# Performance work log

Measured on AMD Instinct MI355X. Metric: run time of the kernel, lower is better.

## Reference

```python
import jax, jax.numpy as jnp
import numpy as np

B, C, H, W = 4, 64, 64, 64
DK, DV = 64, 64


def _conv1x1(x, w, b):
    # x: [B,C,H,W], w: [O,C], b: [O] -> [B,O,H,W]
    return jnp.einsum('bchw,oc->bohw', x, w) + b[None, :, None, None]


def _ordered_mask(N, ordering, dtype):
    mask = jnp.tril(jnp.ones((N, N), dtype=dtype))
    if ordering == 1:
        return mask
    elif ordering == 2:
        return jnp.flip(mask, 1)
    elif ordering == 3:
        return jnp.rot90(mask, 1)
    elif ordering == 4:
        return jnp.flip(jnp.rot90(mask, 1), 0)
    elif ordering == 5:
        return jnp.rot90(mask, 2)
    elif ordering == 6:
        return jnp.flip(jnp.rot90(mask, 2), 1)
    elif ordering == 7:
        return jnp.rot90(mask, 3)
    elif ordering == 8:
        return jnp.flip(jnp.rot90(mask, 3), 1)
    return None


def setup_inputs() -> dict:
    key = jax.random.key(0)
    ks = jax.random.split(key, 9)
    s = 0.02
    return {
        'x': jax.random.normal(ks[0], (B, C, H, W), dtype=jnp.float32),
        'Wq': jax.random.normal(ks[1], (DK, C), dtype=jnp.float32) * s,
        'bq': jnp.zeros((DK,), dtype=jnp.float32),
        'Wk': jax.random.normal(ks[2], (DK, C), dtype=jnp.float32) * s,
        'bk': jnp.zeros((DK,), dtype=jnp.float32),
        'Wv': jax.random.normal(ks[3], (DV, C), dtype=jnp.float32) * s,
        'bv': jnp.zeros((DV,), dtype=jnp.float32),
        'Wo': jax.random.normal(ks[4], (DV, DV + C), dtype=jnp.float32) * s,
        'bo': jnp.zeros((DV,), dtype=jnp.float32),
        'ordering': 1,
    }


def reference(x, Wq, bq, Wk, bk, Wv, bv, Wo, bo, ordering):
    b, c, h, w = x.shape
    N = h * w
    dk, dv = Wq.shape[0], Wv.shape[0]
    Q = _conv1x1(x, Wq, bq).reshape(b, dk, N)  # [B,dk,N]
    K = _conv1x1(x, Wk, bk).reshape(b, dk, N)  # [B,dk,N]
    V = _conv1x1(x, Wv, bv).reshape(b, dv, N)  # [B,dv,N]
    logits = jnp.einsum('bdn,bdm->bnm', Q, K)  # [B,N,N] (no 1/sqrt(dk) scaling, matching source)
    weights = jax.nn.softmax(logits, axis=-1)
    m = _ordered_mask(N, ordering, x.dtype)
    if m is not None:
        weights = weights * m  # post-softmax multiplicative mask
    o = jnp.einsum('bnm,bdm->bdn', weights, V).reshape(b, dv, h, w)
    oc = jnp.concatenate([o, x], axis=1)  # [B,dv+C,H,W]
    return _conv1x1(oc, Wo, bo)
```

## Files before the change

kernel.cpp:

```cpp
#include <hip/hip_runtime.h>

typedef __attribute__((ext_vector_type(8))) short short8;
typedef __attribute__((ext_vector_type(4))) short short4v;
typedef __attribute__((ext_vector_type(4))) float f32x4;
typedef __attribute__((ext_vector_type(16))) float f32x16;
typedef __attribute__((ext_vector_type(4))) unsigned int uint4v;
typedef __attribute__((ext_vector_type(2))) unsigned int uint2v;
typedef unsigned short us;
typedef unsigned int u32;

#define NB 4
#define NC 64
#define NN 4096
#define ND 64
#define LOG2E 1.44269504088896340736f

static __device__ __forceinline__ us f2bf(float x) {
    u32 u = __builtin_bit_cast(u32, x);
    u += 0x7FFFu + ((u >> 16) & 1u);
    return (us)(u >> 16);
}

static __device__ __forceinline__ float bf2f(us v) {
    u32 u = ((u32)v) << 16;
    return __builtin_bit_cast(float, u);
}

static __device__ __forceinline__ u32 cvtpk(float a, float b) {
    u32 r;
    asm("v_cvt_pk_bf16_f32 %0, %1, %2" : "=v"(r) : "v"(a), "v"(b));
    return r;
}

static __device__ __forceinline__ short8 comb(short4v a, short4v b) {
    short8 r;
    r[0] = a[0]; r[1] = a[1]; r[2] = a[2]; r[3] = a[3];
    r[4] = b[0]; r[5] = b[1]; r[6] = b[2]; r[7] = b[3];
    return r;
}

static __device__ __forceinline__ void async_copy16(void* lds, const void* g) {
    __builtin_amdgcn_global_load_lds(
        (const __attribute__((address_space(1))) u32*)g,
        (__attribute__((address_space(3))) u32*)lds, 16, 0, 0);
}

static __device__ __forceinline__ int swz8(int row) {
    return (row & 7) ^ ((row >> 3) & 3);
}

__global__ void cvt_kernel(const float* __restrict__ Wo,
                           const float* __restrict__ Wq,
                           const float* __restrict__ Wk,
                           const float* __restrict__ Wv,
                           us* __restrict__ Wob, us* __restrict__ Wqb,
                           us* __restrict__ Wkb, us* __restrict__ Wvb) {
    int i = blockIdx.x * 256 + threadIdx.x;
    if (i < 8192) Wob[i] = f2bf(Wo[i]);
    else if (i < 12288) Wqb[i - 8192] = f2bf(Wq[i - 8192] * LOG2E);
    else if (i < 16384) Wkb[i - 12288] = f2bf(Wk[i - 12288]);
    else if (i < 20480) Wvb[i - 16384] = f2bf(Wv[i - 16384]);
}

__global__ __launch_bounds__(256) void proj_kernel(
    const float* __restrict__ x,
    const us* __restrict__ Wqb, const float* __restrict__ bq,
    const us* __restrict__ Wkb, const float* __restrict__ bk,
    const us* __restrict__ Wvb, const float* __restrict__ bv,
    us* __restrict__ Qt, us* __restrict__ Kt,
    us* __restrict__ Vm, us* __restrict__ Xbt)
{
    __shared__ float xs[64][64];
    __shared__ __align__(16) us xT[64][64];
    const int t = threadIdx.x;
    const int bid = blockIdx.x;
    const int role = bid & 1;
    const int v = bid >> 1;
    const int b = v >> 6;
    const int n0 = (v & 63) << 6;
    const float* xb = x + (size_t)b * NC * NN + n0;
    #pragma unroll
    for (int i = 0; i < 4; ++i) {
        int s = t + i * 256;
        int c = s >> 4, col = (s & 15) << 2;
        *(f32x4*)&xs[c][col] = *(const f32x4*)&xb[(size_t)c * NN + col];
    }
    __syncthreads();
    {
        int n = t & 63, cg = t >> 6;
        int c0 = cg << 4;
        u32 pk[8];
        #pragma unroll
        for (int j = 0; j < 8; ++j) {
            float a0 = xs[c0 + 2 * j][n], a1 = xs[c0 + 2 * j + 1][n];
            pk[j] = (u32)f2bf(a0) | ((u32)f2bf(a1) << 16);
        }
        int b0 = (cg * 2) ^ (n & 7), b1 = (cg * 2 + 1) ^ (n & 7);
        *(uint4v*)&xT[n][b0 * 8] = (uint4v){pk[0], pk[1], pk[2], pk[3]};
        *(uint4v*)&xT[n][b1 * 8] = (uint4v){pk[4], pk[5], pk[6], pk[7]};
        if (role == 1) {
            us* dst = Xbt + (size_t)(b * NN + n0 + n) * ND + c0;
            *(uint4v*)dst       = (uint4v){pk[0], pk[1], pk[2], pk[3]};
            *(uint4v*)(dst + 8) = (uint4v){pk[4], pk[5], pk[6], pk[7]};
        }
    }
    __syncthreads();
    const int w = t >> 6, l = t & 63, h = l >> 4, ln = l & 15;
    const int row = w * 16 + ln;
    short8 xq0 = *(const short8*)&xT[row][((h ^ (row & 7)) << 3)];
    short8 xq1 = *(const short8*)&xT[row][(((4 + h) ^ (row & 7)) << 3)];

    if (role == 0) {
        #pragma unroll
        for (int p = 0; p < 2; ++p) {
            const us* Wb = p ? Wkb : Wqb;
            const float* bias = p ? bk : bq;
            const float sc = p ? 1.0f : LOG2E;
            us* outp = p ? Kt : Qt;
            #pragma unroll
            for (int di = 0; di < 4; ++di) {
                const int d = di * 16 + ln;
                const us* wrb = Wb + (size_t)d * 64;
                short8 a0 = *(const short8*)(wrb + h * 8);
                short8 a1 = *(const short8*)(wrb + 32 + h * 8);
                f32x4 acc = *(const f32x4*)(bias + di * 16 + h * 4);
                acc *= sc;
                acc = __builtin_amdgcn_mfma_f32_16x16x32_bf16(a0, xq0, acc, 0, 0, 0);
                acc = __builtin_amdgcn_mfma_f32_16x16x32_bf16(a1, xq1, acc, 0, 0, 0);
                u32 lo = (u32)f2bf(acc[0]) | ((u32)f2bf(acc[1]) << 16);
                u32 hi2 = (u32)f2bf(acc[2]) | ((u32)f2bf(acc[3]) << 16);
                *(uint2v*)(outp + (size_t)(b * NN + n0 + row) * ND + di * 16 + h * 4) = (uint2v){lo, hi2};
            }
        }
    } else {
        #pragma unroll
        for (int di = 0; di < 4; ++di) {
            const int d = di * 16 + ln;
            const us* wrb = Wvb + (size_t)d * 64;
            short8 a0 = *(const short8*)(wrb + h * 8);
            short8 a1 = *(const short8*)(wrb + 32 + h * 8);
            f32x4 acc = *(const f32x4*)(bv + di * 16 + h * 4);
            acc = __builtin_amdgcn_mfma_f32_16x16x32_bf16(a0, xq0, acc, 0, 0, 0);
            acc = __builtin_amdgcn_mfma_f32_16x16x32_bf16(a1, xq1, acc, 0, 0, 0);
            us* vp = Vm + (size_t)(b * ND + di * 16 + h * 4) * NN + n0 + row;
            vp[0] = f2bf(acc[0]); vp[NN] = f2bf(acc[1]);
            vp[2 * NN] = f2bf(acc[2]); vp[3 * NN] = f2bf(acc[3]);
        }
    }
}

static __device__ __forceinline__ void mask_bounds32(int pt, int n032, int ng,
    int& lo_n, int& hi_n, int& lo_min, int& lo_max, int& hi_min, int& hi_max)
{
    if (pt == 0)      { lo_n = 0;           hi_n = ng;          lo_min = 0;              lo_max = 0;             hi_min = n032;           hi_max = n032 + 31; }
    else if (pt == 1) { lo_n = NN - 1 - ng; hi_n = NN - 1;      lo_min = NN - 32 - n032; lo_max = NN - 1 - n032; hi_min = NN - 1;         hi_max = NN - 1; }
    else if (pt == 2) { lo_n = ng;          hi_n = NN - 1;      lo_min = n032;           lo_max = n032 + 31;     hi_min = NN - 1;         hi_max = NN - 1; }
    else if (pt == 3) { lo_n = 0;           hi_n = NN - 1 - ng; lo_min = 0;              lo_max = 0;             hi_min = NN - 32 - n032; hi_max = NN - 1 - n032; }
    else              { lo_n = 0;           hi_n = NN - 1;      lo_min = 0;              lo_max = 0;             hi_min = NN - 1;         hi_max = NN - 1; }
}

__global__ __launch_bounds__(512, 4) void attn_kernel(
    const us* __restrict__ Qt, const us* __restrict__ Kt,
    const us* __restrict__ Vm,
    const int* __restrict__ ordp,
    u32* __restrict__ Opk, float* __restrict__ Lb)
{
    __shared__ __align__(16) us Kl[2][64 * 64];
    __shared__ __align__(16) us Vl[2][64 * 64];
    __shared__ float cL[128];

    const int tid = threadIdx.x;
    const int w = tid >> 6, l = tid & 63;
    const int hi = l >> 5, ln = l & 31;
    const int nh = w & 3, mh = w >> 2;
    const int bid = blockIdx.x;
    const int vid = (bid & 7) * 64 + (bid >> 3);
    const int b = vid >> 7;
    const int ms = (vid >> 5) & 3;
    const int qt = vid & 31;
    const int n0 = qt << 7;
    const int mbase = ms << 10;
    const int n032 = n0 + nh * 32;
    const int ng = n032 + ln;

    const int ord = ordp[0];
    int pt = 4;
    if (ord == 1) pt = 0;
    else if (ord == 2 || ord == 3) pt = 1;
    else if (ord == 4 || ord == 5 || ord == 8) pt = 2;
    else if (ord == 6 || ord == 7) pt = 3;
    int lo_n, hi_n, lo_min, lo_max, hi_min, hi_max;
    mask_bounds32(pt, n032, ng, lo_n, hi_n, lo_min, lo_max, hi_min, hi_max);

    const us* kb = Kt + (size_t)b * NN * ND;
    const us* vb = Vm + (size_t)b * ND * NN;
    const us* qrow = Qt + (size_t)(b * NN + n032 + ln) * ND;
    short8 qf0 = *(const short8*)(qrow + 0 * 16 + hi * 8);
    short8 qf1 = *(const short8*)(qrow + 1 * 16 + hi * 8);
    short8 qf2 = *(const short8*)(qrow + 2 * 16 + hi * 8);
    short8 qf3 = *(const short8*)(qrow + 3 * 16 + hi * 8);

    f32x16 O0, O1, Z;
    #pragma unroll
    for (int i = 0; i < 16; ++i) { O0[i] = 0.f; O1[i] = 0.f; Z[i] = 0.f; }
    float Lp = 0.f;

    auto stage = [&](int buf, int t) {
        const int m_base = mbase + t * 64;
        if (w < 4) {
            #pragma unroll
            for (int r = 0; r < 2; ++r) {
                const int rl = w * 16 + r * 8 + (l >> 3);
                const int blk = l & 7;
                const us* src = kb + (size_t)(m_base + rl) * ND + ((blk ^ swz8(rl)) << 3);
                async_copy16(&Kl[buf][(w * 16 + r * 8) * 64], src);
            }
        } else {
            #pragma unroll
            for (int r = 0; r < 2; ++r) {
                const int rl = (w - 4) * 16 + r * 8 + (l >> 3);
                const int blk = l & 7;
                const us* src = vb + (size_t)rl * NN + m_base + ((blk ^ swz8(rl)) << 3);
                async_copy16(&Vl[buf][((w - 4) * 16 + r * 8) * 64], src);
            }
        }
    };

    stage(0, 0);
    for (int t = 0; t < 16; ++t) {
        if (t < 15) {
            stage((t + 1) & 1, t + 1);
            asm volatile("s_waitcnt vmcnt(2)" ::: "memory");
        } else {
            asm volatile("s_waitcnt vmcnt(0)" ::: "memory");
        }
        __builtin_amdgcn_s_barrier();
        __builtin_amdgcn_sched_barrier(0);

        const us* KT = Kl[t & 1];
        const us* VT = Vl[t & 1];
        const int m0s = mbase + t * 64 + mh * 32;
        const bool skip = (m0s + 31 < lo_min) || (m0s > hi_max);
        const bool full = (m0s >= lo_max) && (m0s + 31 <= hi_min);

        __builtin_amdgcn_s_setprio(1);
        {
            const int row = mh * 32 + ln;
            const int rs = swz8(row);
            short8 a0 = *(const short8*)&KT[row * 64 + (((0 + hi) ^ rs) << 3)];
            short8 a1 = *(const short8*)&KT[row * 64 + (((2 + hi) ^ rs) << 3)];
            short8 a2 = *(const short8*)&KT[row * 64 + (((4 + hi) ^ rs) << 3)];
            short8 a3 = *(const short8*)&KT[row * 64 + (((6 + hi) ^ rs) << 3)];
            f32x16 st = __builtin_amdgcn_mfma_f32_32x32x16_bf16(a0, qf0, Z, 0, 0, 0);
            st = __builtin_amdgcn_mfma_f32_32x32x16_bf16(a1, qf1, st, 0, 0, 0);
            st = __builtin_amdgcn_mfma_f32_32x32x16_bf16(a2, qf2, st, 0, 0, 0);
            st = __builtin_amdgcn_mfma_f32_32x32x16_bf16(a3, qf3, st, 0, 0, 0);

            float p[16];
            float lp0 = 0.f, lp1 = 0.f;
            #pragma unroll
            for (int r = 0; r < 16; ++r) {
                p[r] = __builtin_amdgcn_exp2f(st[r]);
                if (r & 1) lp1 += p[r]; else lp0 += p[r];
            }
            Lp += lp0 + lp1;
            if (!skip) {
                if (!full) {
                    #pragma unroll
                    for (int r = 0; r < 16; ++r) {
                        const int mg = m0s + (r & 3) + 8 * (r >> 2) + 4 * hi;
                        if (mg < lo_n || mg > hi_n) p[r] = 0.f;
                    }
                }
                #pragma unroll
                for (int c16 = 0; c16 < 2; ++c16) {
                    uint4v pw;
                    pw[0] = cvtpk(p[c16 * 8 + 0], p[c16 * 8 + 1]);
                    pw[1] = cvtpk(p[c16 * 8 + 2], p[c16 * 8 + 3]);
                    pw[2] = cvtpk(p[c16 * 8 + 4], p[c16 * 8 + 5]);
                    pw[3] = cvtpk(p[c16 * 8 + 6], p[c16 * 8 + 7]);
                    short8 pb = __builtin_bit_cast(short8, pw);
                    const int blkA = mh * 4 + c16 * 2;
                    {
                        const int rv = ln, rvs = swz8(rv);
                        short4v va  = *(const short4v*)&VT[rv * 64 + ((blkA ^ rvs) << 3) + hi * 4];
                        short4v vb2 = *(const short4v*)&VT[rv * 64 + (((blkA + 1) ^ rvs) << 3) + hi * 4];
                        O0 = __builtin_amdgcn_mfma_f32_32x32x16_bf16(comb(va, vb2), pb, O0, 0, 0, 0);
                    }
                    {
                        const int rv = 32 + ln, rvs = swz8(rv);
                        short4v va  = *(const short4v*)&VT[rv * 64 + ((blkA ^ rvs) << 3) + hi * 4];
                        short4v vb2 = *(const short4v*)&VT[rv * 64 + (((blkA + 1) ^ rvs) << 3) + hi * 4];
                        O1 = __builtin_amdgcn_mfma_f32_32x32x16_bf16(comb(va, vb2), pb, O1, 0, 0, 0);
                    }
                }
            }
        }
        __builtin_amdgcn_s_setprio(0);
        __builtin_amdgcn_sched_barrier(0);
        __builtin_amdgcn_s_barrier();
    }

    float Lw = Lp + __shfl_xor(Lp, 32);

    float* cO = (nh < 2 ? (float*)&Kl[0][0] : (float*)&Vl[0][0]) + (nh & 1) * 2048;
    if (mh == 1) {
        float* dsto = cO + ln * 64;
        #pragma unroll
        for (int rq = 0; rq < 4; ++rq) {
            f32x4 s0, s1;
            #pragma unroll
            for (int j = 0; j < 4; ++j) { s0[j] = O0[rq * 4 + j]; s1[j] = O1[rq * 4 + j]; }
            *(f32x4*)&dsto[rq * 8 + hi * 4] = s0;
            *(f32x4*)&dsto[32 + rq * 8 + hi * 4] = s1;
        }
        if (hi == 0) cL[nh * 32 + ln] = Lw;
    }
    __syncthreads();
    if (mh == 1) return;

    const float gL = Lw + cL[nh * 32 + ln];
    const float* sp = cO + ln * 64;
    f32x16 On0 = O0, On1 = O1;
    #pragma unroll
    for (int rq = 0; rq < 4; ++rq) {
        f32x4 a = *(const f32x4*)&sp[rq * 8 + hi * 4];
        f32x4 c = *(const f32x4*)&sp[32 + rq * 8 + hi * 4];
        #pragma unroll
        for (int j = 0; j < 4; ++j) { On0[rq * 4 + j] += a[j]; On1[rq * 4 + j] += c[j]; }
    }

    u32* opk = Opk + ((size_t)(ms * NB + b) * 32) * NN + n032 + ln;
    #pragma unroll
    for (int rp = 0; rp < 16; rp += 2) {
        const int dp = ((rp & 3) >> 1) + 4 * (rp >> 2) + 2 * hi;
        opk[(size_t)dp * NN] = cvtpk(On0[rp], On0[rp + 1]);
        opk[(size_t)(dp + 16) * NN] = cvtpk(On1[rp], On1[rp + 1]);
    }
    if (hi == 0) Lb[(size_t)(ms * NB + b) * NN + n032 + ln] = gL;
}

__global__ __launch_bounds__(64) void combine_kernel(
    const u32* __restrict__ Opk, const float* __restrict__ Lb,
    const us* __restrict__ Xbt, const us* __restrict__ Wob,
    const float* __restrict__ bo, float* __restrict__ out)
{
    const int l = threadIdx.x, hi = l >> 5, ln = l & 31;
    const int gw = blockIdx.x;
    const int b = gw >> 7;
    const int n032 = (gw & 127) << 5;
    const int q = n032 + ln;

    f32x16 On0, On1;
    #pragma unroll
    for (int i = 0; i < 16; ++i) { On0[i] = 0.f; On1[i] = 0.f; }
    #pragma unroll
    for (int part = 0; part < 4; ++part) {
        const u32* pb = Opk + ((size_t)(part * NB + b) * 32) * NN + q;
        #pragma unroll
        for (int rp = 0; rp < 16; rp += 2) {
            const int dp = ((rp & 3) >> 1) + 4 * (rp >> 2) + 2 * hi;
            u32 w0 = pb[(size_t)dp * NN];
            u32 w1 = pb[(size_t)(dp + 16) * NN];
            On0[rp]     += bf2f((us)(w0 & 0xFFFFu));
            On0[rp + 1] += bf2f((us)(w0 >> 16));
            On1[rp]     += bf2f((us)(w1 & 0xFFFFu));
            On1[rp + 1] += bf2f((us)(w1 >> 16));
        }
    }
    float gL = 0.f;
    #pragma unroll
    for (int i = 0; i < 4; ++i) gL += Lb[(size_t)(i * NB + b) * NN + q];
    const float rl2 = 1.0f / gL;
    #pragma unroll
    for (int i = 0; i < 16; ++i) { On0[i] *= rl2; On1[i] *= rl2; }

    short8 Bf[8];
    {
        uint4v w0, w1, w2, w3;
        w0[0] = cvtpk(On0[0], On0[1]);   w0[1] = cvtpk(On0[2], On0[3]);
        w0[2] = cvtpk(On0[4], On0[5]);   w0[3] = cvtpk(On0[6], On0[7]);
        w1[0] = cvtpk(On0[8], On0[9]);   w1[1] = cvtpk(On0[10], On0[11]);
        w1[2] = cvtpk(On0[12], On0[13]); w1[3] = cvtpk(On0[14], On0[15]);
        w2[0] = cvtpk(On1[0], On1[1]);   w2[1] = cvtpk(On1[2], On1[3]);
        w2[2] = cvtpk(On1[4], On1[5]);   w2[3] = cvtpk(On1[6], On1[7]);
        w3[0] = cvtpk(On1[8], On1[9]);   w3[1] = cvtpk(On1[10], On1[11]);
        w3[2] = cvtpk(On1[12], On1[13]); w3[3] = cvtpk(On1[14], On1[15]);
        Bf[0] = __builtin_bit_cast(short8, w0);
        Bf[1] = __builtin_bit_cast(short8, w1);
        Bf[2] = __builtin_bit_cast(short8, w2);
        Bf[3] = __builtin_bit_cast(short8, w3);
    }
    const us* xrow = Xbt + (size_t)(b * NN + q) * ND;
    #pragma unroll
    for (int c4 = 0; c4 < 4; ++c4)
        Bf[4 + c4] = comb(*(const short4v*)(xrow + c4 * 16 + hi * 4),
                          *(const short4v*)(xrow + c4 * 16 + hi * 4 + 8));

    f32x16 acc0, acc1;
    #pragma unroll
    for (int rq = 0; rq < 4; ++rq) {
        f32x4 b0 = *(const f32x4*)&bo[rq * 8 + hi * 4];
        f32x4 b1 = *(const f32x4*)&bo[32 + rq * 8 + hi * 4];
        #pragma unroll
        for (int j = 0; j < 4; ++j) { acc0[rq * 4 + j] = b0[j]; acc1[rq * 4 + j] = b1[j]; }
    }
    const us* wr0 = Wob + (size_t)ln * 128;
    const us* wr1 = Wob + (size_t)(32 + ln) * 128;
    #pragma unroll
    for (int kc = 0; kc < 8; ++kc) {
        short8 wf0 = comb(*(const short4v*)(wr0 + kc * 16 + hi * 4),
                          *(const short4v*)(wr0 + kc * 16 + hi * 4 + 8));
        short8 wf1 = comb(*(const short4v*)(wr1 + kc * 16 + hi * 4),
                          *(const short4v*)(wr1 + kc * 16 + hi * 4 + 8));
        acc0 = __builtin_amdgcn_mfma_f32_32x32x16_bf16(wf0, Bf[kc], acc0, 0, 0, 0);
        acc1 = __builtin_amdgcn_mfma_f32_32x32x16_bf16(wf1, Bf[kc], acc1, 0, 0, 0);
    }
    #pragma unroll
    for (int r = 0; r < 16; ++r) {
        const int od = (r & 3) + 8 * (r >> 2) + 4 * hi;
        out[((size_t)b * 64 + od) * NN + q] = acc0[r];
        out[((size_t)b * 64 + 32 + od) * NN + q] = acc1[r];
    }
}

extern "C" void kernel_launch(void* const* d_in, const int* in_sizes, int n_in,
                              void* d_out, int out_size, void* d_ws, size_t ws_size,
                              hipStream_t stream) {
    (void)in_sizes; (void)n_in; (void)out_size; (void)ws_size;
    const float* x  = (const float*)d_in[0];
    const float* Wq = (const float*)d_in[1];
    const float* bq = (const float*)d_in[2];
    const float* Wk = (const float*)d_in[3];
    const float* bk = (const float*)d_in[4];
    const float* Wv = (const float*)d_in[5];
    const float* bv = (const float*)d_in[6];
    const float* Wo = (const float*)d_in[7];
    const float* bo = (const float*)d_in[8];
    const int* ord  = (const int*)d_in[9];
    float* out = (float*)d_out;

    us* Qt  = (us*)d_ws;
    us* Kt  = Qt  + (size_t)NB * NN * ND;
    us* Vm  = Kt  + (size_t)NB * NN * ND;
    us* Xbt = Vm  + (size_t)NB * NN * ND;
    us* Wob = Xbt + (size_t)NB * NN * ND;
    u32* Opk = (u32*)(Wob + ND * (ND + NC));
    float* Lb = (float*)(Opk + (size_t)16 * 32 * NN);
    us* Wqb = (us*)(Lb + (size_t)4 * NB * NN);
    us* Wkb = Wqb + 4096;
    us* Wvb = Wkb + 4096;

    cvt_kernel<<<dim3(80), dim3(256), 0, stream>>>(Wo, Wq, Wk, Wv, Wob, Wqb, Wkb, Wvb);
    proj_kernel<<<dim3(NB * 64 * 2), dim3(256), 0, stream>>>(
        x, Wqb, bq, Wkb, bk, Wvb, bv, Qt, Kt, Vm, Xbt);
    attn_kernel<<<dim3(512), dim3(512), 0, stream>>>(Qt, Kt, Vm, ord, Opk, Lb);
    combine_kernel<<<dim3(512), dim3(64), 0, stream>>>(Opk, Lb, Xbt, Wob, bo, out);
}
```

Baseline: 52.97 us.

## Repack K/V into MFMA fragment layout and read directly from global without LDS

Adds a repack kernel that rewrites K and V into per-32-key tiles already in MFMA operand order. The attention kernel then loads fragments straight from global memory (L2-cached) instead of staging them through double-buffered LDS with barriers. Each wave now independently handles one 32-query group over one of eight key splits, which removes the intra-block LDS reduction. The combine kernel sums eight partials instead of four. The cost is an extra kernel launch, twice the partial-output traffic, and reliance on cache hits for the K/V reuse that LDS used to provide.

```diff
diff --git a/kernel.cpp b/kernel.cpp
--- a/kernel.cpp
+++ b/kernel.cpp
@@ -37,16 +37,6 @@
     r[0] = a[0]; r[1] = a[1]; r[2] = a[2]; r[3] = a[3];
     r[4] = b[0]; r[5] = b[1]; r[6] = b[2]; r[7] = b[3];
     return r;
-}
-
-static __device__ __forceinline__ void async_copy16(void* lds, const void* g) {
-    __builtin_amdgcn_global_load_lds(
-        (const __attribute__((address_space(1))) u32*)g,
-        (__attribute__((address_space(3))) u32*)lds, 16, 0, 0);
-}
-
-static __device__ __forceinline__ int swz8(int row) {
-    return (row & 7) ^ ((row >> 3) & 3);
 }
 
 __global__ void cvt_kernel(const float* __restrict__ Wo,
@@ -149,6 +139,31 @@
     }
 }
 
+__global__ __launch_bounds__(256) void repack_kernel(
+    const us* __restrict__ Kt, const us* __restrict__ Vm,
+    us* __restrict__ Kf, us* __restrict__ Vf)
+{
+    const int bid = blockIdx.x;
+    const int b = bid >> 7, mt = bid & 127;
+    const int t = threadIdx.x;
+    const int l = t & 63, s = t >> 6;
+    {
+        const int row = mt * 32 + (l & 31);
+        const int d0 = s * 16 + (l >> 5) * 8;
+        uint4v v = *(const uint4v*)(Kt + ((size_t)b * NN + row) * ND + d0);
+        *(uint4v*)(Kf + ((size_t)(b * 128 + mt) * 2048) + s * 512 + l * 8) = v;
+    }
+    {
+        const int dh = s >> 1, c16 = s & 1;
+        const int d = dh * 32 + (l & 31);
+        const int m0 = mt * 32 + c16 * 16 + (l >> 5) * 4;
+        const us* src = Vm + ((size_t)b * ND + d) * NN + m0;
+        short4v a = *(const short4v*)src;
+        short4v c = *(const short4v*)(src + 8);
+        *(short8*)(Vf + ((size_t)(b * 128 + mt) * 2048) + s * 512 + l * 8) = comb(a, c);
+    }
+}
+
 static __device__ __forceinline__ void mask_bounds32(int pt, int n032, int ng,
     int& lo_n, int& hi_n, int& lo_min, int& lo_max, int& hi_min, int& hi_max)
 {
@@ -159,29 +174,23 @@
     else              { lo_n = 0;           hi_n = NN - 1;      lo_min = 0;              lo_max = 0;             hi_min = NN - 1;         hi_max = NN - 1; }
 }
 
-__global__ __launch_bounds__(512, 4) void attn_kernel(
-    const us* __restrict__ Qt, const us* __restrict__ Kt,
-    const us* __restrict__ Vm,
+__global__ __launch_bounds__(256, 4) void attn_kernel(
+    const us* __restrict__ Qt, const us* __restrict__ Kf,
+    const us* __restrict__ Vf,
     const int* __restrict__ ordp,
     u32* __restrict__ Opk, float* __restrict__ Lb)
 {
-    __shared__ __align__(16) us Kl[2][64 * 64];
-    __shared__ __align__(16) us Vl[2][64 * 64];
-    __shared__ float cL[128];
-
     const int tid = threadIdx.x;
     const int w = tid >> 6, l = tid & 63;
     const int hi = l >> 5, ln = l & 31;
-    const int nh = w & 3, mh = w >> 2;
     const int bid = blockIdx.x;
-    const int vid = (bid & 7) * 64 + (bid >> 3);
-    const int b = vid >> 7;
-    const int ms = (vid >> 5) & 3;
-    const int qt = vid & 31;
-    const int n0 = qt << 7;
-    const int mbase = ms << 10;
-    const int n032 = n0 + nh * 32;
-    const int ng = n032 + ln;
+    const int vid = (bid & 7) * 128 + (bid >> 3);
+    const int W = vid * 4 + w;
+    const int combo = W >> 7;
+    const int b = combo >> 3, ms = combo & 7;
+    const int qg = W & 127;
+    const int q0 = qg << 5;
+    const int ng = q0 + ln;
 
     const int ord = ordp[0];
     int pt = 4;
@@ -190,11 +199,9 @@
     else if (ord == 4 || ord == 5 || ord == 8) pt = 2;
     else if (ord == 6 || ord == 7) pt = 3;
     int lo_n, hi_n, lo_min, lo_max, hi_min, hi_max;
-    mask_bounds32(pt, n032, ng, lo_n, hi_n, lo_min, lo_max, hi_min, hi_max);
-
-    const us* kb = Kt + (size_t)b * NN * ND;
-    const us* vb = Vm + (size_t)b * ND * NN;
-    const us* qrow = Qt + (size_t)(b * NN + n032 + ln) * ND;
+    mask_bounds32(pt, q0, ng, lo_n, hi_n, lo_min, lo_max, hi_min, hi_max);
+
+    const us* qrow = Qt + (size_t)(b * NN + q0 + ln) * ND;
     short8 qf0 = *(const short8*)(qrow + 0 * 16 + hi * 8);
     short8 qf1 = *(const short8*)(qrow + 1 * 16 + hi * 8);
     short8 qf2 = *(const short8*)(qrow + 2 * 16 + hi * 8);
@@ -205,139 +212,68 @@
     for (int i = 0; i < 16; ++i) { O0[i] = 0.f; O1[i] = 0.f; Z[i] = 0.f; }
     float Lp = 0.f;
 
-    auto stage = [&](int buf, int t) {
-        const int m_base = mbase + t * 64;
-        if (w < 4) {
-            #pragma unroll
-            for (int r = 0; r < 2; ++r) {
-                const int rl = w * 16 + r * 8 + (l >> 3);
-                const int blk = l & 7;
-                const us* src = kb + (size_t)(m_base + rl) * ND + ((blk ^ swz8(rl)) << 3);
-                async_copy16(&Kl[buf][(w * 16 + r * 8) * 64], src);
-            }
-        } else {
-            #pragma unroll
-            for (int r = 0; r < 2; ++r) {
-                const int rl = (w - 4) * 16 + r * 8 + (l >> 3);
-                const int blk = l & 7;
-                const us* src = vb + (size_t)rl * NN + m_base + ((blk ^ swz8(rl)) << 3);
-                async_copy16(&Vl[buf][((w - 4) * 16 + r * 8) * 64], src);
-            }
-        }
-    };
-
-    stage(0, 0);
+    const us* kfb = Kf + (size_t)(b * 128 + ms * 16) * 2048;
+    const us* vfb = Vf + (size_t)(b * 128 + ms * 16) * 2048;
+
+    #pragma unroll 2
     for (int t = 0; t < 16; ++t) {
-        if (t < 15) {
-            stage((t + 1) & 1, t + 1);
-            asm volatile("s_waitcnt vmcnt(2)" ::: "memory");
-        } else {
-            asm volatile("s_waitcnt vmcnt(0)" ::: "memory");
-        }
-        __builtin_amdgcn_s_barrier();
-        __builtin_amdgcn_sched_barrier(0);
-
-        const us* KT = Kl[t & 1];
-        const us* VT = Vl[t & 1];
-        const int m0s = mbase + t * 64 + mh * 32;
+        const us* kt = kfb + t * 2048 + l * 8;
+        short8 a0 = *(const short8*)(kt);
+        short8 a1 = *(const short8*)(kt + 512);
+        short8 a2 = *(const short8*)(kt + 1024);
+        short8 a3 = *(const short8*)(kt + 1536);
+        const int m0s = (ms * 16 + t) * 32;
         const bool skip = (m0s + 31 < lo_min) || (m0s > hi_max);
         const bool full = (m0s >= lo_max) && (m0s + 31 <= hi_min);
 
-        __builtin_amdgcn_s_setprio(1);
-        {
-            const int row = mh * 32 + ln;
-            const int rs = swz8(row);
-            short8 a0 = *(const short8*)&KT[row * 64 + (((0 + hi) ^ rs) << 3)];
-            short8 a1 = *(const short8*)&KT[row * 64 + (((2 + hi) ^ rs) << 3)];
-            short8 a2 = *(const short8*)&KT[row * 64 + (((4 + hi) ^ rs) << 3)];
-            short8 a3 = *(const short8*)&KT[row * 64 + (((6 + hi) ^ rs) << 3)];
-            f32x16 st = __builtin_amdgcn_mfma_f32_32x32x16_bf16(a0, qf0, Z, 0, 0, 0);
-            st = __builtin_amdgcn_mfma_f32_32x32x16_bf16(a1, qf1, st, 0, 0, 0);
-            st = __builtin_amdgcn_mfma_f32_32x32x16_bf16(a2, qf2, st, 0, 0, 0);
-            st = __builtin_amdgcn_mfma_f32_32x32x16_bf16(a3, qf3, st, 0, 0, 0);
-
-            float p[16];
-            float lp0 = 0.f, lp1 = 0.f;
-            #pragma unroll
-            for (int r = 0; r < 16; ++r) {
-                p[r] = __builtin_amdgcn_exp2f(st[r]);
-                if (r & 1) lp1 += p[r]; else lp0 += p[r];
-            }
-            Lp += lp0 + lp1;
-            if (!skip) {
-                if (!full) {
-                    #pragma unroll
-                    for (int r = 0; r < 16; ++r) {
-                        const int mg = m0s + (r & 3) + 8 * (r >> 2) + 4 * hi;
-                        if (mg < lo_n || mg > hi_n) p[r] = 0.f;
-                    }
-                }
+        f32x16 st = __builtin_amdgcn_mfma_f32_32x32x16_bf16(a0, qf0, Z, 0, 0, 0);
+        st = __builtin_amdgcn_mfma_f32_32x32x16_bf16(a1, qf1, st, 0, 0, 0);
+        st = __builtin_amdgcn_mfma_f32_32x32x16_bf16(a2, qf2, st, 0, 0, 0);
+        st = __builtin_amdgcn_mfma_f32_32x32x16_bf16(a3, qf3, st, 0, 0, 0);
+
+        float p[16];
+        float lp0 = 0.f, lp1 = 0.f;
+        #pragma unroll
+        for (int r = 0; r < 16; ++r) {
+            p[r] = __builtin_amdgcn_exp2f(st[r]);
+            if (r & 1) lp1 += p[r]; else lp0 += p[r];
+        }
+        Lp += lp0 + lp1;
+        if (!skip) {
+            if (!full) {
                 #pragma unroll
-                for (int c16 = 0; c16 < 2; ++c16) {
-                    uint4v pw;
-                    pw[0] = cvtpk(p[c16 * 8 + 0], p[c16 * 8 + 1]);
-                    pw[1] = cvtpk(p[c16 * 8 + 2], p[c16 * 8 + 3]);
-                    pw[2] = cvtpk(p[c16 * 8 + 4], p[c16 * 8 + 5]);
-                    pw[3] = cvtpk(p[c16 * 8 + 6], p[c16 * 8 + 7]);
-                    short8 pb = __builtin_bit_cast(short8, pw);
-                    const int blkA = mh * 4 + c16 * 2;
-                    {
-                        const int rv = ln, rvs = swz8(rv);
-                        short4v va  = *(const short4v*)&VT[rv * 64 + ((blkA ^ rvs) << 3) + hi * 4];
-                        short4v vb2 = *(const short4v*)&VT[rv * 64 + (((blkA + 1) ^ rvs) << 3) + hi * 4];
-                        O0 = __builtin_amdgcn_mfma_f32_32x32x16_bf16(comb(va, vb2), pb, O0, 0, 0, 0);
-                    }
-                    {
-                        const int rv = 32 + ln, rvs = swz8(rv);
-                        short4v va  = *(const short4v*)&VT[rv * 64 + ((blkA ^ rvs) << 3) + hi * 4];
-                        short4v vb2 = *(const short4v*)&VT[rv * 64 + (((blkA + 1) ^ rvs) << 3) + hi * 4];
-                        O1 = __builtin_amdgcn_mfma_f32_32x32x16_bf16(comb(va, vb2), pb, O1, 0, 0, 0);
-                    }
+                for (int r = 0; r < 16; ++r) {
+                    const int mg = m0s + (r & 3) + 8 * (r >> 2) + 4 * hi;
+                    if (mg < lo_n || mg > hi_n) p[r] = 0.f;
                 }
             }
-        }
-        __builtin_amdgcn_s_setprio(0);
-        __builtin_amdgcn_sched_barrier(0);
-        __builtin_amdgcn_s_barrier();
+            const us* vt = vfb + t * 2048 + l * 8;
+            #pragma unroll
+            for (int c16 = 0; c16 < 2; ++c16) {
+                uint4v pw;
+                pw[0] = cvtpk(p[c16 * 8 + 0], p[c16 * 8 + 1]);
+                pw[1] = cvtpk(p[c16 * 8 + 2], p[c16 * 8 + 3]);
+                pw[2] = cvtpk(p[c16 * 8 + 4], p[c16 * 8 + 5]);
+                pw[3] = cvtpk(p[c16 * 8 + 6], p[c16 * 8 + 7]);
+                short8 pb = __builtin_bit_cast(short8, pw);
+                short8 v0 = *(const short8*)(vt + (0 * 2 + c16) * 512);
+                short8 v1 = *(const short8*)(vt + (1 * 2 + c16) * 512);
+                O0 = __builtin_amdgcn_mfma_f32_32x32x16_bf16(v0, pb, O0, 0, 0, 0);
+                O1 = __builtin_amdgcn_mfma_f32_32x32x16_bf16(v1, pb, O1, 0, 0, 0);
+            }
+        }
     }
 
     float Lw = Lp + __shfl_xor(Lp, 32);
 
-    float* cO = (nh < 2 ? (float*)&Kl[0][0] : (float*)&Vl[0][0]) + (nh & 1) * 2048;
-    if (mh == 1) {
-        float* dsto = cO + ln * 64;
-        #pragma unroll
-        for (int rq = 0; rq < 4; ++rq) {
-            f32x4 s0, s1;
-            #pragma unroll
-            for (int j = 0; j < 4; ++j) { s0[j] = O0[rq * 4 + j]; s1[j] = O1[rq * 4 + j]; }
-            *(f32x4*)&dsto[rq * 8 + hi * 4] = s0;
-            *(f32x4*)&dsto[32 + rq * 8 + hi * 4] = s1;
-        }
-        if (hi == 0) cL[nh * 32 + ln] = Lw;
-    }
-    __syncthreads();
-    if (mh == 1) return;
-
-    const float gL = Lw + cL[nh * 32 + ln];
-    const float* sp = cO + ln * 64;
-    f32x16 On0 = O0, On1 = O1;
-    #pragma unroll
-    for (int rq = 0; rq < 4; ++rq) {
-        f32x4 a = *(const f32x4*)&sp[rq * 8 + hi * 4];
-        f32x4 c = *(const f32x4*)&sp[32 + rq * 8 + hi * 4];
-        #pragma unroll
-        for (int j = 0; j < 4; ++j) { On0[rq * 4 + j] += a[j]; On1[rq * 4 + j] += c[j]; }
-    }
-
-    u32* opk = Opk + ((size_t)(ms * NB + b) * 32) * NN + n032 + ln;
+    u32* opk = Opk + ((size_t)(ms * NB + b) * 32) * NN + q0 + ln;
     #pragma unroll
     for (int rp = 0; rp < 16; rp += 2) {
         const int dp = ((rp & 3) >> 1) + 4 * (rp >> 2) + 2 * hi;
-        opk[(size_t)dp * NN] = cvtpk(On0[rp], On0[rp + 1]);
-        opk[(size_t)(dp + 16) * NN] = cvtpk(On1[rp], On1[rp + 1]);
-    }
-    if (hi == 0) Lb[(size_t)(ms * NB + b) * NN + n032 + ln] = gL;
+        opk[(size_t)dp * NN] = cvtpk(O0[rp], O0[rp + 1]);
+        opk[(size_t)(dp + 16) * NN] = cvtpk(O1[rp], O1[rp + 1]);
+    }
+    if (hi == 0) Lb[(size_t)(ms * NB + b) * NN + q0 + ln] = Lw;
 }
 
 __global__ __launch_bounds__(64) void combine_kernel(
@@ -355,7 +291,7 @@
     #pragma unroll
     for (int i = 0; i < 16; ++i) { On0[i] = 0.f; On1[i] = 0.f; }
     #pragma unroll
-    for (int part = 0; part < 4; ++part) {
+    for (int part = 0; part < 8; ++part) {
         const u32* pb = Opk + ((size_t)(part * NB + b) * 32) * NN + q;
         #pragma unroll
         for (int rp = 0; rp < 16; rp += 2) {
@@ -370,7 +306,7 @@
     }
     float gL = 0.f;
     #pragma unroll
-    for (int i = 0; i < 4; ++i) gL += Lb[(size_t)(i * NB + b) * NN + q];
+    for (int i = 0; i < 8; ++i) gL += Lb[(size_t)(i * NB + b) * NN + q];
     const float rl2 = 1.0f / gL;
     #pragma unroll
     for (int i = 0; i < 16; ++i) { On0[i] *= rl2; On1[i] *= rl2; }
@@ -445,15 +381,18 @@
     us* Vm  = Kt  + (size_t)NB * NN * ND;
     us* Xbt = Vm  + (size_t)NB * NN * ND;
     us* Wob = Xbt + (size_t)NB * NN * ND;
-    u32* Opk = (u32*)(Wob + ND * (ND + NC));
-    float* Lb = (float*)(Opk + (size_t)16 * 32 * NN);
-    us* Wqb = (us*)(Lb + (size_t)4 * NB * NN);
+    us* Kf  = Wob + ND * (ND + NC);
+    us* Vf  = Kf + (size_t)NB * 128 * 2048;
+    u32* Opk = (u32*)(Vf + (size_t)NB * 128 * 2048);
+    float* Lb = (float*)(Opk + (size_t)8 * NB * 32 * NN);
+    us* Wqb = (us*)(Lb + (size_t)8 * NB * NN);
     us* Wkb = Wqb + 4096;
     us* Wvb = Wkb + 4096;
 
     cvt_kernel<<<dim3(80), dim3(256), 0, stream>>>(Wo, Wq, Wk, Wv, Wob, Wqb, Wkb, Wvb);
     proj_kernel<<<dim3(NB * 64 * 2), dim3(256), 0, stream>>>(
         x, Wqb, bq, Wkb, bk, Wvb, bv, Qt, Kt, Vm, Xbt);
-    attn_kernel<<<dim3(512), dim3(512), 0, stream>>>(Qt, Kt, Vm, ord, Opk, Lb);
+    repack_kernel<<<dim3(512), dim3(256), 0, stream>>>(Kt, Vm, Kf, Vf);
+    attn_kernel<<<dim3(1024), dim3(256), 0, stream>>>(Qt, Kf, Vf, ord, Opk, Lb);
     combine_kernel<<<dim3(512), dim3(64), 0, stream>>>(Opk, Lb, Xbt, Wob, bo, out);
 }
```

After: 58.83 us. 1.11x slower.

## Pre-pack K and V into MFMA fragment order for contiguous LDS loads

Applied to the files above, without the earlier changes.

Adds a repack kernel that rewrites K and V into a per-32-row tile layout already in MFMA operand order. The attention kernel can then stage tiles with plain contiguous async copies and read each fragment with a single 16-byte LDS load, with no XOR swizzle and no combining of two 8-byte reads. The cost is an extra kernel launch plus an extra global read and write pass over K and V. Because each lane now reads a consecutive 16-byte chunk, the old swizzle is no longer needed to avoid LDS bank conflicts.

```diff
diff --git a/kernel.cpp b/kernel.cpp
--- a/kernel.cpp
+++ b/kernel.cpp
@@ -43,10 +43,6 @@
     __builtin_amdgcn_global_load_lds(
         (const __attribute__((address_space(1))) u32*)g,
         (__attribute__((address_space(3))) u32*)lds, 16, 0, 0);
-}
-
-static __device__ __forceinline__ int swz8(int row) {
-    return (row & 7) ^ ((row >> 3) & 3);
 }
 
 __global__ void cvt_kernel(const float* __restrict__ Wo,
@@ -149,6 +145,31 @@
     }
 }
 
+__global__ __launch_bounds__(256) void repack_kernel(
+    const us* __restrict__ Kt, const us* __restrict__ Vm,
+    us* __restrict__ Kf, us* __restrict__ Vf)
+{
+    const int bid = blockIdx.x;
+    const int b = bid >> 7, mt = bid & 127;
+    const int t = threadIdx.x;
+    const int l = t & 63, s = t >> 6;
+    {
+        const int row = mt * 32 + (l & 31);
+        const int d0 = s * 16 + (l >> 5) * 8;
+        uint4v v = *(const uint4v*)(Kt + ((size_t)b * NN + row) * ND + d0);
+        *(uint4v*)(Kf + ((size_t)(b * 128 + mt) * 2048) + s * 512 + l * 8) = v;
+    }
+    {
+        const int dh = s >> 1, c16 = s & 1;
+        const int d = dh * 32 + (l & 31);
+        const int m0 = mt * 32 + c16 * 16 + (l >> 5) * 4;
+        const us* src = Vm + ((size_t)b * ND + d) * NN + m0;
+        short4v a = *(const short4v*)src;
+        short4v c = *(const short4v*)(src + 8);
+        *(short8*)(Vf + ((size_t)(b * 128 + mt) * 2048) + s * 512 + l * 8) = comb(a, c);
+    }
+}
+
 static __device__ __forceinline__ void mask_bounds32(int pt, int n032, int ng,
     int& lo_n, int& hi_n, int& lo_min, int& lo_max, int& hi_min, int& hi_max)
 {
@@ -160,13 +181,13 @@
 }
 
 __global__ __launch_bounds__(512, 4) void attn_kernel(
-    const us* __restrict__ Qt, const us* __restrict__ Kt,
-    const us* __restrict__ Vm,
+    const us* __restrict__ Qt, const us* __restrict__ Kf,
+    const us* __restrict__ Vf,
     const int* __restrict__ ordp,
     u32* __restrict__ Opk, float* __restrict__ Lb)
 {
-    __shared__ __align__(16) us Kl[2][64 * 64];
-    __shared__ __align__(16) us Vl[2][64 * 64];
+    __shared__ __align__(16) us Kl[2][4096];
+    __shared__ __align__(16) us Vl[2][4096];
     __shared__ float cL[128];
 
     const int tid = threadIdx.x;
@@ -192,8 +213,6 @@
     int lo_n, hi_n, lo_min, lo_max, hi_min, hi_max;
     mask_bounds32(pt, n032, ng, lo_n, hi_n, lo_min, lo_max, hi_min, hi_max);
 
-    const us* kb = Kt + (size_t)b * NN * ND;
-    const us* vb = Vm + (size_t)b * ND * NN;
     const us* qrow = Qt + (size_t)(b * NN + n032 + ln) * ND;
     short8 qf0 = *(const short8*)(qrow + 0 * 16 + hi * 8);
     short8 qf1 = *(const short8*)(qrow + 1 * 16 + hi * 8);
@@ -205,23 +224,20 @@
     for (int i = 0; i < 16; ++i) { O0[i] = 0.f; O1[i] = 0.f; Z[i] = 0.f; }
     float Lp = 0.f;
 
+    const size_t fbase = (size_t)(b * 128 + (mbase >> 5)) * 2048;
     auto stage = [&](int buf, int t) {
-        const int m_base = mbase + t * 64;
+        const size_t tb = fbase + (size_t)t * 4096;
         if (w < 4) {
             #pragma unroll
             for (int r = 0; r < 2; ++r) {
-                const int rl = w * 16 + r * 8 + (l >> 3);
-                const int blk = l & 7;
-                const us* src = kb + (size_t)(m_base + rl) * ND + ((blk ^ swz8(rl)) << 3);
-                async_copy16(&Kl[buf][(w * 16 + r * 8) * 64], src);
+                const int ch = 2 * w + r;
+                async_copy16(&Kl[buf][ch * 512], Kf + tb + ch * 512 + l * 8);
             }
         } else {
             #pragma unroll
             for (int r = 0; r < 2; ++r) {
-                const int rl = (w - 4) * 16 + r * 8 + (l >> 3);
-                const int blk = l & 7;
-                const us* src = vb + (size_t)rl * NN + m_base + ((blk ^ swz8(rl)) << 3);
-                async_copy16(&Vl[buf][((w - 4) * 16 + r * 8) * 64], src);
+                const int ch = 2 * (w - 4) + r;
+                async_copy16(&Vl[buf][ch * 512], Vf + tb + ch * 512 + l * 8);
             }
         }
     };
@@ -237,20 +253,18 @@
         __builtin_amdgcn_s_barrier();
         __builtin_amdgcn_sched_barrier(0);
 
-        const us* KT = Kl[t & 1];
-        const us* VT = Vl[t & 1];
+        const us* KT = &Kl[t & 1][mh * 2048 + l * 8];
+        const us* VT = &Vl[t & 1][mh * 2048 + l * 8];
         const int m0s = mbase + t * 64 + mh * 32;
         const bool skip = (m0s + 31 < lo_min) || (m0s > hi_max);
         const bool full = (m0s >= lo_max) && (m0s + 31 <= hi_min);
 
         __builtin_amdgcn_s_setprio(1);
         {
-            const int row = mh * 32 + ln;
-            const int rs = swz8(row);
-            short8 a0 = *(const short8*)&KT[row * 64 + (((0 + hi) ^ rs) << 3)];
-            short8 a1 = *(const short8*)&KT[row * 64 + (((2 + hi) ^ rs) << 3)];
-            short8 a2 = *(const short8*)&KT[row * 64 + (((4 + hi) ^ rs) << 3)];
-            short8 a3 = *(const short8*)&KT[row * 64 + (((6 + hi) ^ rs) << 3)];
+            short8 a0 = *(const short8*)(KT);
+            short8 a1 = *(const short8*)(KT + 512);
+            short8 a2 = *(const short8*)(KT + 1024);
+            short8 a3 = *(const short8*)(KT + 1536);
             f32x16 st = __builtin_amdgcn_mfma_f32_32x32x16_bf16(a0, qf0, Z, 0, 0, 0);
             st = __builtin_amdgcn_mfma_f32_32x32x16_bf16(a1, qf1, st, 0, 0, 0);
             st = __builtin_amdgcn_mfma_f32_32x32x16_bf16(a2, qf2, st, 0, 0, 0);
@@ -280,19 +294,10 @@
                     pw[2] = cvtpk(p[c16 * 8 + 4], p[c16 * 8 + 5]);
                     pw[3] = cvtpk(p[c16 * 8 + 6], p[c16 * 8 + 7]);
                     short8 pb = __builtin_bit_cast(short8, pw);
-                    const int blkA = mh * 4 + c16 * 2;
-                    {
-                        const int rv = ln, rvs = swz8(rv);
-                        short4v va  = *(const short4v*)&VT[rv * 64 + ((blkA ^ rvs) << 3) + hi * 4];
-                        short4v vb2 = *(const short4v*)&VT[rv * 64 + (((blkA + 1) ^ rvs) << 3) + hi * 4];
-                        O0 = __builtin_amdgcn_mfma_f32_32x32x16_bf16(comb(va, vb2), pb, O0, 0, 0, 0);
-                    }
-                    {
-                        const int rv = 32 + ln, rvs = swz8(rv);
-                        short4v va  = *(const short4v*)&VT[rv * 64 + ((blkA ^ rvs) << 3) + hi * 4];
-                        short4v vb2 = *(const short4v*)&VT[rv * 64 + (((blkA + 1) ^ rvs) << 3) + hi * 4];
-                        O1 = __builtin_amdgcn_mfma_f32_32x32x16_bf16(comb(va, vb2), pb, O1, 0, 0, 0);
-                    }
+                    short8 v0 = *(const short8*)(VT + (0 * 2 + c16) * 512);
+                    short8 v1 = *(const short8*)(VT + (1 * 2 + c16) * 512);
+                    O0 = __builtin_amdgcn_mfma_f32_32x32x16_bf16(v0, pb, O0, 0, 0, 0);
+                    O1 = __builtin_amdgcn_mfma_f32_32x32x16_bf16(v1, pb, O1, 0, 0, 0);
                 }
             }
         }
@@ -445,8 +450,10 @@
     us* Vm  = Kt  + (size_t)NB * NN * ND;
     us* Xbt = Vm  + (size_t)NB * NN * ND;
     us* Wob = Xbt + (size_t)NB * NN * ND;
-    u32* Opk = (u32*)(Wob + ND * (ND + NC));
-    float* Lb = (float*)(Opk + (size_t)16 * 32 * NN);
+    us* Kf  = Wob + ND * (ND + NC);
+    us* Vf  = Kf + (size_t)NB * 128 * 2048;
+    u32* Opk = (u32*)(Vf + (size_t)NB * 128 * 2048);
+    float* Lb = (float*)(Opk + (size_t)4 * NB * 32 * NN);
     us* Wqb = (us*)(Lb + (size_t)4 * NB * NN);
     us* Wkb = Wqb + 4096;
     us* Wvb = Wkb + 4096;
@@ -454,6 +461,7 @@
     cvt_kernel<<<dim3(80), dim3(256), 0, stream>>>(Wo, Wq, Wk, Wv, Wob, Wqb, Wkb, Wvb);
     proj_kernel<<<dim3(NB * 64 * 2), dim3(256), 0, stream>>>(
         x, Wqb, bq, Wkb, bk, Wvb, bv, Qt, Kt, Vm, Xbt);
-    attn_kernel<<<dim3(512), dim3(512), 0, stream>>>(Qt, Kt, Vm, ord, Opk, Lb);
+    repack_kernel<<<dim3(512), dim3(256), 0, stream>>>(Kt, Vm, Kf, Vf);
+    attn_kernel<<<dim3(512), dim3(512), 0, stream>>>(Qt, Kf, Vf, ord, Opk, Lb);
     combine_kernel<<<dim3(512), dim3(64), 0, stream>>>(Opk, Lb, Xbt, Wob, bo, out);
 }
```

Result: slower. 55.20 us (+4.2%).

## Halve attention block to 4 waves looping both key halves, merge projection roles

Applied to the files above, without the earlier changes.

The attention kernel drops from 8 to 4 waves per block. Each wave now walks both 32-key halves of every tile itself, so the shared-memory reduction of partial O and L across the m-halves and its extra barrier go away. The QK^T chain is split into two independent accumulators that are summed before exp2, to shorten the MFMA dependency chain. The projection kernel stops splitting Q/K and V work into two block roles: one block now computes Q, K, V and Xbt, which halves the grid and avoids staging x twice. The cost is less parallelism per block and more serial work per wave.

```diff
diff --git a/kernel.cpp b/kernel.cpp
--- a/kernel.cpp
+++ b/kernel.cpp
@@ -73,9 +73,7 @@
     __shared__ float xs[64][64];
     __shared__ __align__(16) us xT[64][64];
     const int t = threadIdx.x;
-    const int bid = blockIdx.x;
-    const int role = bid & 1;
-    const int v = bid >> 1;
+    const int v = blockIdx.x;
     const int b = v >> 6;
     const int n0 = (v & 63) << 6;
     const float* xb = x + (size_t)b * NC * NN + n0;
@@ -98,11 +96,9 @@
         int b0 = (cg * 2) ^ (n & 7), b1 = (cg * 2 + 1) ^ (n & 7);
         *(uint4v*)&xT[n][b0 * 8] = (uint4v){pk[0], pk[1], pk[2], pk[3]};
         *(uint4v*)&xT[n][b1 * 8] = (uint4v){pk[4], pk[5], pk[6], pk[7]};
-        if (role == 1) {
-            us* dst = Xbt + (size_t)(b * NN + n0 + n) * ND + c0;
-            *(uint4v*)dst       = (uint4v){pk[0], pk[1], pk[2], pk[3]};
-            *(uint4v*)(dst + 8) = (uint4v){pk[4], pk[5], pk[6], pk[7]};
-        }
+        us* dst = Xbt + (size_t)(b * NN + n0 + n) * ND + c0;
+        *(uint4v*)dst       = (uint4v){pk[0], pk[1], pk[2], pk[3]};
+        *(uint4v*)(dst + 8) = (uint4v){pk[4], pk[5], pk[6], pk[7]};
     }
     __syncthreads();
     const int w = t >> 6, l = t & 63, h = l >> 4, ln = l & 15;
@@ -110,42 +106,39 @@
     short8 xq0 = *(const short8*)&xT[row][((h ^ (row & 7)) << 3)];
     short8 xq1 = *(const short8*)&xT[row][(((4 + h) ^ (row & 7)) << 3)];
 
-    if (role == 0) {
-        #pragma unroll
-        for (int p = 0; p < 2; ++p) {
-            const us* Wb = p ? Wkb : Wqb;
-            const float* bias = p ? bk : bq;
-            const float sc = p ? 1.0f : LOG2E;
-            us* outp = p ? Kt : Qt;
-            #pragma unroll
-            for (int di = 0; di < 4; ++di) {
-                const int d = di * 16 + ln;
-                const us* wrb = Wb + (size_t)d * 64;
-                short8 a0 = *(const short8*)(wrb + h * 8);
-                short8 a1 = *(const short8*)(wrb + 32 + h * 8);
-                f32x4 acc = *(const f32x4*)(bias + di * 16 + h * 4);
-                acc *= sc;
-                acc = __builtin_amdgcn_mfma_f32_16x16x32_bf16(a0, xq0, acc, 0, 0, 0);
-                acc = __builtin_amdgcn_mfma_f32_16x16x32_bf16(a1, xq1, acc, 0, 0, 0);
-                u32 lo = (u32)f2bf(acc[0]) | ((u32)f2bf(acc[1]) << 16);
-                u32 hi2 = (u32)f2bf(acc[2]) | ((u32)f2bf(acc[3]) << 16);
-                *(uint2v*)(outp + (size_t)(b * NN + n0 + row) * ND + di * 16 + h * 4) = (uint2v){lo, hi2};
-            }
-        }
-    } else {
+    #pragma unroll
+    for (int p = 0; p < 2; ++p) {
+        const us* Wb = p ? Wkb : Wqb;
+        const float* bias = p ? bk : bq;
+        const float sc = p ? 1.0f : LOG2E;
+        us* outp = p ? Kt : Qt;
         #pragma unroll
         for (int di = 0; di < 4; ++di) {
             const int d = di * 16 + ln;
-            const us* wrb = Wvb + (size_t)d * 64;
+            const us* wrb = Wb + (size_t)d * 64;
             short8 a0 = *(const short8*)(wrb + h * 8);
             short8 a1 = *(const short8*)(wrb + 32 + h * 8);
-            f32x4 acc = *(const f32x4*)(bv + di * 16 + h * 4);
+            f32x4 acc = *(const f32x4*)(bias + di * 16 + h * 4);
+            acc *= sc;
             acc = __builtin_amdgcn_mfma_f32_16x16x32_bf16(a0, xq0, acc, 0, 0, 0);
             acc = __builtin_amdgcn_mfma_f32_16x16x32_bf16(a1, xq1, acc, 0, 0, 0);
-            us* vp = Vm + (size_t)(b * ND + di * 16 + h * 4) * NN + n0 + row;
-            vp[0] = f2bf(acc[0]); vp[NN] = f2bf(acc[1]);
-            vp[2 * NN] = f2bf(acc[2]); vp[3 * NN] = f2bf(acc[3]);
-        }
+            u32 lo = (u32)f2bf(acc[0]) | ((u32)f2bf(acc[1]) << 16);
+            u32 hi2 = (u32)f2bf(acc[2]) | ((u32)f2bf(acc[3]) << 16);
+            *(uint2v*)(outp + (size_t)(b * NN + n0 + row) * ND + di * 16 + h * 4) = (uint2v){lo, hi2};
+        }
+    }
+    #pragma unroll
+    for (int di = 0; di < 4; ++di) {
+        const int d = di * 16 + ln;
+        const us* wrb = Wvb + (size_t)d * 64;
+        short8 a0 = *(const short8*)(wrb + h * 8);
+        short8 a1 = *(const short8*)(wrb + 32 + h * 8);
+        f32x4 acc = *(const f32x4*)(bv + di * 16 + h * 4);
+        acc = __builtin_amdgcn_mfma_f32_16x16x32_bf16(a0, xq0, acc, 0, 0, 0);
+        acc = __builtin_amdgcn_mfma_f32_16x16x32_bf16(a1, xq1, acc, 0, 0, 0);
+        us* vp = Vm + (size_t)(b * ND + di * 16 + h * 4) * NN + n0 + row;
+        vp[0] = f2bf(acc[0]); vp[NN] = f2bf(acc[1]);
+        vp[2 * NN] = f2bf(acc[2]); vp[3 * NN] = f2bf(acc[3]);
     }
 }
 
@@ -159,7 +152,7 @@
     else              { lo_n = 0;           hi_n = NN - 1;      lo_min = 0;              lo_max = 0;             hi_min = NN - 1;         hi_max = NN - 1; }
 }
 
-__global__ __launch_bounds__(512, 4) void attn_kernel(
+__global__ __launch_bounds__(256, 4) void attn_kernel(
     const us* __restrict__ Qt, const us* __restrict__ Kt,
     const us* __restrict__ Vm,
     const int* __restrict__ ordp,
@@ -167,12 +160,11 @@
 {
     __shared__ __align__(16) us Kl[2][64 * 64];
     __shared__ __align__(16) us Vl[2][64 * 64];
-    __shared__ float cL[128];
 
     const int tid = threadIdx.x;
     const int w = tid >> 6, l = tid & 63;
     const int hi = l >> 5, ln = l & 31;
-    const int nh = w & 3, mh = w >> 2;
+    const int nh = w;
     const int bid = blockIdx.x;
     const int vid = (bid & 7) * 64 + (bid >> 3);
     const int b = vid >> 7;
@@ -207,21 +199,21 @@
 
     auto stage = [&](int buf, int t) {
         const int m_base = mbase + t * 64;
-        if (w < 4) {
+        if (w < 2) {
             #pragma unroll
-            for (int r = 0; r < 2; ++r) {
-                const int rl = w * 16 + r * 8 + (l >> 3);
+            for (int r = 0; r < 4; ++r) {
+                const int rl = w * 32 + r * 8 + (l >> 3);
                 const int blk = l & 7;
                 const us* src = kb + (size_t)(m_base + rl) * ND + ((blk ^ swz8(rl)) << 3);
-                async_copy16(&Kl[buf][(w * 16 + r * 8) * 64], src);
+                async_copy16(&Kl[buf][(w * 32 + r * 8) * 64], src);
             }
         } else {
             #pragma unroll
-            for (int r = 0; r < 2; ++r) {
-                const int rl = (w - 4) * 16 + r * 8 + (l >> 3);
+            for (int r = 0; r < 4; ++r) {
+                const int rl = (w - 2) * 32 + r * 8 + (l >> 3);
                 const int blk = l & 7;
                 const us* src = vb + (size_t)rl * NN + m_base + ((blk ^ swz8(rl)) << 3);
-                async_copy16(&Vl[buf][((w - 4) * 16 + r * 8) * 64], src);
+                async_copy16(&Vl[buf][((w - 2) * 32 + r * 8) * 64], src);
             }
         }
     };
@@ -230,7 +222,7 @@
     for (int t = 0; t < 16; ++t) {
         if (t < 15) {
             stage((t + 1) & 1, t + 1);
-            asm volatile("s_waitcnt vmcnt(2)" ::: "memory");
+            asm volatile("s_waitcnt vmcnt(4)" ::: "memory");
         } else {
             asm volatile("s_waitcnt vmcnt(0)" ::: "memory");
         }
@@ -239,28 +231,30 @@
 
         const us* KT = Kl[t & 1];
         const us* VT = Vl[t & 1];
-        const int m0s = mbase + t * 64 + mh * 32;
-        const bool skip = (m0s + 31 < lo_min) || (m0s > hi_max);
-        const bool full = (m0s >= lo_max) && (m0s + 31 <= hi_min);
 
         __builtin_amdgcn_s_setprio(1);
-        {
-            const int row = mh * 32 + ln;
+        #pragma unroll
+        for (int s01 = 0; s01 < 2; ++s01) {
+            const int m0s = mbase + t * 64 + s01 * 32;
+            const bool skip = (m0s + 31 < lo_min) || (m0s > hi_max);
+            const bool full = (m0s >= lo_max) && (m0s + 31 <= hi_min);
+
+            const int row = s01 * 32 + ln;
             const int rs = swz8(row);
             short8 a0 = *(const short8*)&KT[row * 64 + (((0 + hi) ^ rs) << 3)];
             short8 a1 = *(const short8*)&KT[row * 64 + (((2 + hi) ^ rs) << 3)];
             short8 a2 = *(const short8*)&KT[row * 64 + (((4 + hi) ^ rs) << 3)];
             short8 a3 = *(const short8*)&KT[row * 64 + (((6 + hi) ^ rs) << 3)];
-            f32x16 st = __builtin_amdgcn_mfma_f32_32x32x16_bf16(a0, qf0, Z, 0, 0, 0);
-            st = __builtin_amdgcn_mfma_f32_32x32x16_bf16(a1, qf1, st, 0, 0, 0);
-            st = __builtin_amdgcn_mfma_f32_32x32x16_bf16(a2, qf2, st, 0, 0, 0);
-            st = __builtin_amdgcn_mfma_f32_32x32x16_bf16(a3, qf3, st, 0, 0, 0);
+            f32x16 st0 = __builtin_amdgcn_mfma_f32_32x32x16_bf16(a0, qf0, Z, 0, 0, 0);
+            f32x16 st1 = __builtin_amdgcn_mfma_f32_32x32x16_bf16(a2, qf2, Z, 0, 0, 0);
+            st0 = __builtin_amdgcn_mfma_f32_32x32x16_bf16(a1, qf1, st0, 0, 0, 0);
+            st1 = __builtin_amdgcn_mfma_f32_32x32x16_bf16(a3, qf3, st1, 0, 0, 0);
 
             float p[16];
             float lp0 = 0.f, lp1 = 0.f;
             #pragma unroll
             for (int r = 0; r < 16; ++r) {
-                p[r] = __builtin_amdgcn_exp2f(st[r]);
+                p[r] = __builtin_amdgcn_exp2f(st0[r] + st1[r]);
                 if (r & 1) lp1 += p[r]; else lp0 += p[r];
             }
             Lp += lp0 + lp1;
@@ -280,7 +274,7 @@
                     pw[2] = cvtpk(p[c16 * 8 + 4], p[c16 * 8 + 5]);
                     pw[3] = cvtpk(p[c16 * 8 + 6], p[c16 * 8 + 7]);
                     short8 pb = __builtin_bit_cast(short8, pw);
-                    const int blkA = mh * 4 + c16 * 2;
+                    const int blkA = s01 * 4 + c16 * 2;
                     {
                         const int rv = ln, rvs = swz8(rv);
                         short4v va  = *(const short4v*)&VT[rv * 64 + ((blkA ^ rvs) << 3) + hi * 4];
@@ -303,41 +297,14 @@
 
     float Lw = Lp + __shfl_xor(Lp, 32);
 
-    float* cO = (nh < 2 ? (float*)&Kl[0][0] : (float*)&Vl[0][0]) + (nh & 1) * 2048;
-    if (mh == 1) {
-        float* dsto = cO + ln * 64;
-        #pragma unroll
-        for (int rq = 0; rq < 4; ++rq) {
-            f32x4 s0, s1;
-            #pragma unroll
-            for (int j = 0; j < 4; ++j) { s0[j] = O0[rq * 4 + j]; s1[j] = O1[rq * 4 + j]; }
-            *(f32x4*)&dsto[rq * 8 + hi * 4] = s0;
-            *(f32x4*)&dsto[32 + rq * 8 + hi * 4] = s1;
-        }
-        if (hi == 0) cL[nh * 32 + ln] = Lw;
-    }
-    __syncthreads();
-    if (mh == 1) return;
-
-    const float gL = Lw + cL[nh * 32 + ln];
-    const float* sp = cO + ln * 64;
-    f32x16 On0 = O0, On1 = O1;
-    #pragma unroll
-    for (int rq = 0; rq < 4; ++rq) {
-        f32x4 a = *(const f32x4*)&sp[rq * 8 + hi * 4];
-        f32x4 c = *(const f32x4*)&sp[32 + rq * 8 + hi * 4];
-        #pragma unroll
-        for (int j = 0; j < 4; ++j) { On0[rq * 4 + j] += a[j]; On1[rq * 4 + j] += c[j]; }
-    }
-
     u32* opk = Opk + ((size_t)(ms * NB + b) * 32) * NN + n032 + ln;
     #pragma unroll
     for (int rp = 0; rp < 16; rp += 2) {
         const int dp = ((rp & 3) >> 1) + 4 * (rp >> 2) + 2 * hi;
-        opk[(size_t)dp * NN] = cvtpk(On0[rp], On0[rp + 1]);
-        opk[(size_t)(dp + 16) * NN] = cvtpk(On1[rp], On1[rp + 1]);
-    }
-    if (hi == 0) Lb[(size_t)(ms * NB + b) * NN + n032 + ln] = gL;
+        opk[(size_t)dp * NN] = cvtpk(O0[rp], O0[rp + 1]);
+        opk[(size_t)(dp + 16) * NN] = cvtpk(O1[rp], O1[rp + 1]);
+    }
+    if (hi == 0) Lb[(size_t)(ms * NB + b) * NN + n032 + ln] = Lw;
 }
 
 __global__ __launch_bounds__(64) void combine_kernel(
@@ -452,8 +419,8 @@
     us* Wvb = Wkb + 4096;
 
     cvt_kernel<<<dim3(80), dim3(256), 0, stream>>>(Wo, Wq, Wk, Wv, Wob, Wqb, Wkb, Wvb);
-    proj_kernel<<<dim3(NB * 64 * 2), dim3(256), 0, stream>>>(
+    proj_kernel<<<dim3(NB * 64), dim3(256), 0, stream>>>(
         x, Wqb, bq, Wkb, bk, Wvb, bv, Qt, Kt, Vm, Xbt);
-    attn_kernel<<<dim3(512), dim3(512), 0, stream>>>(Qt, Kt, Vm, ord, Opk, Lb);
+    attn_kernel<<<dim3(512), dim3(256), 0, stream>>>(Qt, Kt, Vm, ord, Opk, Lb);
     combine_kernel<<<dim3(512), dim3(64), 0, stream>>>(Opk, Lb, Xbt, Wob, bo, out);
 }
```

Result: slower. 69.35 us (+30.9%).
